# Kernel tuning notes

Hardware: AMD Instinct MI355X
Metric: run time of the kernel (lower is better)

## Reference

```python
import jax, jax.numpy as jnp
import numpy as np

M = 2          # interp_dim
D = 4          # interp_degree
MESH_LOWER = np.array([0.0, 0.0], dtype=np.float32)
MESH_UPPER = np.array([1.0, 1.0], dtype=np.float32)
MESH_SIZE = np.array([64, 64], dtype=np.int32)   # coe grid = mesh_size*D+1 = [257, 257]


def _lagrange_basis(t):
    """t: [N, M] local coordinate in [0, D]; returns bases [N, M, D+1].
    L_j(t) = prod_{k != j} (t - k) / (j - k)."""
    ks = jnp.arange(D + 1, dtype=t.dtype)
    tk = t[..., None] - ks                       # [N, M, D+1]
    bs = []
    for j in range(D + 1):                       # small fixed loop over D+1=5 bases
        num = jnp.ones(t.shape, t.dtype)
        denom = 1.0
        for k in range(D + 1):
            if k != j:
                num = num * tk[..., k]
                denom *= float(j - k)
        bs.append(num / denom)
    return jnp.stack(bs, axis=-1)                # [N, M, D+1]


def setup_inputs() -> dict:
    key = jax.random.key(0)
    k1, k2 = jax.random.split(key)
    inputs = jax.random.uniform(k1, (2048, 2048, M), dtype=jnp.float32)  # points in [0,1)^2
    grid = tuple(int(s) * D + 1 for s in MESH_SIZE)                      # (257, 257)
    interp_coe = jax.random.normal(k2, grid, dtype=jnp.float32)
    return {"inputs": inputs, "interp_coe": interp_coe}


def reference(inputs, interp_coe):
    size = inputs.shape
    x = inputs.reshape(-1, M)                                   # [N, M]
    lower = jnp.asarray(MESH_LOWER, x.dtype)
    upper = jnp.asarray(MESH_UPPER, x.dtype)
    msize = jnp.asarray(MESH_SIZE.astype(np.float32), x.dtype)
    u = (x - lower) / (upper - lower) * msize                   # grid coordinates
    cell = jnp.clip(jnp.floor(u), 0.0, msize - 1.0)             # [N, M] element index
    t = (u - cell) * D                                          # local coord in [0, D]
    basis = _lagrange_basis(t)                                  # [N, M, D+1]
    base = cell.astype(jnp.int32) * D                           # [N, M] global node base index
    offs = jnp.arange(D + 1, dtype=jnp.int32)
    i0 = base[:, 0, None] + offs                                # [N, D+1]
    i1 = base[:, 1, None] + offs                                # [N, D+1]
    coe = interp_coe[i0[:, :, None], i1[:, None, :]]            # [N, D+1, D+1] gathered cell coes
    out = jnp.einsum('nij,ni,nj->n', coe, basis[:, 0], basis[:, 1])
    return out.reshape(size[:-1])
```

## Files before the change

kernel.cpp:

```cpp
#include <hip/hip_runtime.h>

#define NGRID 257
#define LDS_PITCH 260
#define LDS_BYTES (LDS_PITCH * NGRID * 2)
#define BLOCK 1024
#define GRID 256
#define ITERS 8

typedef _Float16 half4_t __attribute__((ext_vector_type(4)));
typedef float    f2v     __attribute__((ext_vector_type(2)));

struct __attribute__((packed, aligned(4))) f4u { float x, y, z, w; };

struct PtFrag {
    half4_t lo[5];
    half4_t hi[5];
};

__device__ __forceinline__ void lag_basis(float t, float b[5]) {
    float f0 = t;
    float f1 = t - 1.0f;
    float f2 = t - 2.0f;
    float f3 = t - 3.0f;
    float f4 = t - 4.0f;
    float p01 = f0 * f1;
    float p12 = f1 * f2;
    float p23 = f2 * f3;
    float p34 = f3 * f4;
    b[0] = p12 * p34 * (1.0f / 24.0f);
    b[1] = f0 * f2 * p34 * (-1.0f / 6.0f);
    b[2] = p01 * p34 * (1.0f / 4.0f);
    b[3] = p01 * f2 * f4 * (-1.0f / 6.0f);
    b[4] = p01 * p23 * (1.0f / 24.0f);
}

__device__ __forceinline__ int pt_off(float x0, float x1) {
    float u0 = x0 * 64.0f, u1 = x1 * 64.0f;
    float c0 = fminf(fmaxf(floorf(u0), 0.0f), 63.0f);
    float c1 = fminf(fmaxf(floorf(u1), 0.0f), 63.0f);
    return ((int)c0 * 4) * LDS_PITCH + ((int)c1 * 4);
}

__device__ __forceinline__ void stage_point(const _Float16* __restrict__ lds,
                                            int off, PtFrag& f) {
    const _Float16* base = lds + off;
#pragma unroll
    for (int i = 0; i < 5; ++i) {
        const _Float16* rp = base + i * LDS_PITCH;
        f.lo[i] = *(const half4_t*)rp;
        f.hi[i] = *(const half4_t*)(rp + 4);
    }
}

__device__ __forceinline__ float eval_pt(const PtFrag& f, float x0, float x1) {
    float u0 = x0 * 64.0f, u1 = x1 * 64.0f;
    float c0 = fminf(fmaxf(floorf(u0), 0.0f), 63.0f);
    float c1 = fminf(fmaxf(floorf(u1), 0.0f), 63.0f);
    float b0[5], b1[5];
    lag_basis((u0 - c0) * 4.0f, b0);
    lag_basis((u1 - c1) * 4.0f, b1);
    float acc = 0.0f;
#pragma unroll
    for (int i = 0; i < 5; ++i) {
        float rd = (float)f.lo[i][0] * b1[0];
        rd = fmaf((float)f.lo[i][1], b1[1], rd);
        rd = fmaf((float)f.lo[i][2], b1[2], rd);
        rd = fmaf((float)f.lo[i][3], b1[3], rd);
        rd = fmaf((float)f.hi[i][0], b1[4], rd);
        acc = fmaf(b0[i], rd, acc);
    }
    return acc;
}

__launch_bounds__(BLOCK, 4)
__global__ void lagrange_kernel(const float* __restrict__ inputs,
                                const float* __restrict__ coe,
                                float* __restrict__ out,
                                int npairs) {
    extern __shared__ _Float16 lds[];

    for (int g = threadIdx.x; g < NGRID * 65; g += BLOCK) {
        int r = g / 65;
        int c4 = (g - r * 65) * 4;
        if (c4 < 256) {
            f4u q = *(const f4u*)(coe + r * NGRID + c4);
            half4_t h = { (_Float16)q.x, (_Float16)q.y,
                          (_Float16)q.z, (_Float16)q.w };
            *(half4_t*)(lds + r * LDS_PITCH + c4) = h;
        } else {
            lds[r * LDS_PITCH + 256] = (_Float16)coe[r * NGRID + 256];
        }
    }
    __syncthreads();

    const float4* __restrict__ in4 = (const float4*)inputs;
    f2v* __restrict__ out2 = (f2v*)out;
    const int tid = blockIdx.x * BLOCK + threadIdx.x;
    const int stride = GRID * BLOCK;
    (void)npairs;

    float4 va, vb, vc;
    PtFrag fA[2], fB[2];

    va = in4[tid];
    vb = in4[tid + stride];
    stage_point(lds, pt_off(va.x, va.y), fA[0]);
    stage_point(lds, pt_off(va.z, va.w), fB[0]);

#pragma unroll
    for (int k = 0; k < ITERS; ++k) {
        if (k + 2 < ITERS) vc = in4[tid + (k + 2) * stride];
        if (k + 1 < ITERS) {
            stage_point(lds, pt_off(vb.x, vb.y), fA[(k + 1) & 1]);
            stage_point(lds, pt_off(vb.z, vb.w), fB[(k + 1) & 1]);
        }
        f2v r;
        r.x = eval_pt(fA[k & 1], va.x, va.y);
        r.y = eval_pt(fB[k & 1], va.z, va.w);
        __builtin_nontemporal_store(r, &out2[tid + k * stride]);
        va = vb;
        vb = vc;
    }
}

extern "C" void kernel_launch(void* const* d_in, const int* in_sizes, int n_in,
                              void* d_out, int out_size, void* d_ws, size_t ws_size,
                              hipStream_t stream) {
    const float* inputs = (const float*)d_in[0];
    const float* coe    = (const float*)d_in[1];
    float* out = (float*)d_out;
    int npairs = out_size >> 1;

    (void)hipFuncSetAttribute((const void*)lagrange_kernel,
                              hipFuncAttributeMaxDynamicSharedMemorySize,
                              LDS_BYTES);

    dim3 grid(GRID), block(BLOCK);
    hipLaunchKernelGGL(lagrange_kernel, grid, block, LDS_BYTES, stream,
                       inputs, coe, out, npairs);
}
```

Measured before the change: 97.99 us.

## Process one point per thread per iteration with 3-stage LDS prefetch pipeline

Each thread now handles one point per iteration over 16 iterations instead of two points per iteration over 8, loading float2 inputs and storing scalar outputs. The LDS staging keeps three point fragments in rotation, so fetches run two iterations ahead while input loads run three ahead. The high part of each row now loads only a half2 instead of a half4, which cuts LDS traffic and registers per point. In exchange, global loads and stores become narrower (8-byte loads, 4-byte stores), which may reduce memory efficiency.

Measured after the change: 94.82 us. 1.03x faster.

```diff
diff --git a/kernel.cpp b/kernel.cpp
--- a/kernel.cpp
+++ b/kernel.cpp
@@ -5,16 +5,16 @@
 #define LDS_BYTES (LDS_PITCH * NGRID * 2)
 #define BLOCK 1024
 #define GRID 256
-#define ITERS 8
+#define ITERS 16
 
+typedef _Float16 half2_t __attribute__((ext_vector_type(2)));
 typedef _Float16 half4_t __attribute__((ext_vector_type(4)));
-typedef float    f2v     __attribute__((ext_vector_type(2)));
 
 struct __attribute__((packed, aligned(4))) f4u { float x, y, z, w; };
 
 struct PtFrag {
     half4_t lo[5];
-    half4_t hi[5];
+    half2_t hi[5];
 };
 
 __device__ __forceinline__ void lag_basis(float t, float b[5]) {
@@ -45,11 +45,11 @@
                                             int off, PtFrag& f) {
     const _Float16* base = lds + off;
 #pragma unroll
-    for (int i = 0; i < 5; ++i) {
-        const _Float16* rp = base + i * LDS_PITCH;
-        f.lo[i] = *(const half4_t*)rp;
-        f.hi[i] = *(const half4_t*)(rp + 4);
-    }
+    for (int i = 0; i < 5; ++i)
+        f.lo[i] = *(const half4_t*)(base + i * LDS_PITCH);
+#pragma unroll
+    for (int i = 0; i < 5; ++i)
+        f.hi[i] = *(const half2_t*)(base + i * LDS_PITCH + 4);
 }
 
 __device__ __forceinline__ float eval_pt(const PtFrag& f, float x0, float x1) {
@@ -76,7 +76,7 @@
 __global__ void lagrange_kernel(const float* __restrict__ inputs,
                                 const float* __restrict__ coe,
                                 float* __restrict__ out,
-                                int npairs) {
+                                int npts) {
     extern __shared__ _Float16 lds[];
 
     for (int g = threadIdx.x; g < NGRID * 65; g += BLOCK) {
@@ -93,33 +93,29 @@
     }
     __syncthreads();
 
-    const float4* __restrict__ in4 = (const float4*)inputs;
-    f2v* __restrict__ out2 = (f2v*)out;
+    const float2* __restrict__ in2 = (const float2*)inputs;
     const int tid = blockIdx.x * BLOCK + threadIdx.x;
     const int stride = GRID * BLOCK;
-    (void)npairs;
+    (void)npts;
 
-    float4 va, vb, vc;
-    PtFrag fA[2], fB[2];
+    float2 w0, w1, w2, w3;
+    PtFrag f[3];
 
-    va = in4[tid];
-    vb = in4[tid + stride];
-    stage_point(lds, pt_off(va.x, va.y), fA[0]);
-    stage_point(lds, pt_off(va.z, va.w), fB[0]);
+    w0 = in2[tid];
+    w1 = in2[tid + stride];
+    w2 = in2[tid + 2 * stride];
+    stage_point(lds, pt_off(w0.x, w0.y), f[0]);
+    stage_point(lds, pt_off(w1.x, w1.y), f[1]);
 
 #pragma unroll
     for (int k = 0; k < ITERS; ++k) {
-        if (k + 2 < ITERS) vc = in4[tid + (k + 2) * stride];
-        if (k + 1 < ITERS) {
-            stage_point(lds, pt_off(vb.x, vb.y), fA[(k + 1) & 1]);
-            stage_point(lds, pt_off(vb.z, vb.w), fB[(k + 1) & 1]);
-        }
-        f2v r;
-        r.x = eval_pt(fA[k & 1], va.x, va.y);
-        r.y = eval_pt(fB[k & 1], va.z, va.w);
-        __builtin_nontemporal_store(r, &out2[tid + k * stride]);
-        va = vb;
-        vb = vc;
+        if (k + 3 < ITERS) w3 = in2[tid + (k + 3) * stride];
+        if (k + 2 < ITERS) stage_point(lds, pt_off(w2.x, w2.y), f[(k + 2) % 3]);
+        float r = eval_pt(f[k % 3], w0.x, w0.y);
+        __builtin_nontemporal_store(r, &out[tid + k * stride]);
+        w0 = w1;
+        w1 = w2;
+        w2 = w3;
     }
 }
 
@@ -129,7 +125,7 @@
     const float* inputs = (const float*)d_in[0];
     const float* coe    = (const float*)d_in[1];
     float* out = (float*)d_out;
-    int npairs = out_size >> 1;
+    int npts = out_size;
 
     (void)hipFuncSetAttribute((const void*)lagrange_kernel,
                               hipFuncAttributeMaxDynamicSharedMemorySize,
@@ -137,5 +133,5 @@
 
     dim3 grid(GRID), block(BLOCK);
     hipLaunchKernelGGL(lagrange_kernel, grid, block, LDS_BYTES, stream,
-                       inputs, coe, out, npairs);
+                       inputs, coe, out, npts);
 }
```
